# Performance work log

Measured on AMD Instinct MI355X. Metric: run time of the kernel, lower is better.

## Reference

```python
import jax, jax.numpy as jnp
import numpy as np

EPS = 1e-5
NUM_HEADS = 16


def _rmsnorm(x, w, eps=EPS):
    var = jnp.mean(jnp.square(x), axis=-1, keepdims=True)
    return x * jax.lax.rsqrt(var + eps) * w


def setup_inputs() -> dict:
    key = jax.random.key(0)
    ks = jax.random.split(key, 7)
    B, T, H = 4, 8192, 1024
    KD, VD = 512, 1024          # key_dim = 0.5*H, value_dim = H
    hk, hv = KD // NUM_HEADS, VD // NUM_HEADS  # 32, 64
    return {
        "hidden_states": jax.random.normal(ks[0], (B, T, H), jnp.float32),
        "recurrent_state": jax.random.normal(ks[1], (B, NUM_HEADS, hk, hv), jnp.float32),
        "norm_w": jax.random.uniform(ks[2], (H,), jnp.float32, 0.5, 1.5),
        "q_w": jax.random.normal(ks[3], (KD, H), jnp.float32) * 0.02,
        "v_norm_w": jax.random.uniform(ks[4], (hv,), jnp.float32, 0.5, 1.5),
        "o_w": jax.random.normal(ks[5], (H, VD), jnp.float32) * 0.02,
        "gate_w": jax.random.normal(ks[6], (H, H), jnp.float32) * 0.02,
    }


def reference(hidden_states, recurrent_state, norm_w, q_w, v_norm_w, o_w, gate_w):
    B, T, H = hidden_states.shape
    nh = NUM_HEADS
    x = _rmsnorm(hidden_states, norm_w)                      # [B,T,H]
    q = (x @ q_w.T).reshape(B, T, nh, -1)                    # [B,T,h,dk]
    # F.normalize(dim=-1): divide by max(L2 norm, 1e-12)
    q = q / jnp.maximum(jnp.linalg.norm(q, axis=-1, keepdims=True), 1e-12)
    o = jnp.einsum('bthk,bhkv->bthv', q, recurrent_state)    # [B,T,h,dv]
    o = _rmsnorm(o, v_norm_w)
    o = o.reshape(B, T, -1) @ o_w.T                          # [B,T,H]
    gate = jax.nn.sigmoid(x @ gate_w.T)                      # [B,T,H]
    return gate * o
```

## Files before the change

kernel.cpp:

```cpp
#include <hip/hip_runtime.h>
#include <hip/hip_bf16.h>
#include <stdint.h>

typedef __attribute__((ext_vector_type(8))) short short8;
typedef __attribute__((ext_vector_type(4))) float floatx4;
typedef __attribute__((ext_vector_type(2))) unsigned int uint2v;

#define DEV static __device__ __forceinline__
#define FENCE() asm volatile("" ::: "memory")

DEV unsigned short f2bs(float f) {
  union { float f; unsigned u; } v; v.f = f;
  unsigned u = v.u;
  u += 0x7fffu + ((u >> 16) & 1u);
  return (unsigned short)(u >> 16);
}
DEV float bs2f(unsigned short s) {
  union { unsigned u; float f; } v; v.u = ((unsigned)s) << 16;
  return v.f;
}
DEV unsigned pack2(float a, float b) {
  return (unsigned)f2bs(a) | ((unsigned)f2bs(b) << 16);
}

DEV void gload_lds16(const void* g, void* l) {
  __builtin_amdgcn_global_load_lds(
      (const __attribute__((address_space(1))) void*)g,
      (__attribute__((address_space(3))) void*)l, 16, 0, 0);
}

static constexpr int Hdim = 1024;
static constexpr int KDim = 512;
static constexpr int NH = 16;
static constexpr int HK = 32;
static constexpr int HV = 64;
static constexpr int Mtok = 4 * 8192;

__global__ __launch_bounds__(256) void k_cvt(const float4* __restrict__ in,
                                             uint2v* __restrict__ out, int n4) {
  int i = blockIdx.x * 256 + threadIdx.x;
  if (i >= n4) return;
  float4 v = in[i];
  uint2v o;
  o.x = pack2(v.x, v.y);
  o.y = pack2(v.z, v.w);
  out[i] = o;
}

__global__ __launch_bounds__(256) void k_cvts(const float* __restrict__ S,
                                              unsigned short* __restrict__ St) {
  int i = blockIdx.x * 256 + threadIdx.x;
  if (i >= 4 * NH * HV * HK) return;
  int k = i & 31, v = (i >> 5) & 63, bh = i >> 11;
  St[i] = f2bs(S[(size_t)(bh * HK + k) * HV + v]);
}

__global__ __launch_bounds__(256) void k_rmsnorm(const float* __restrict__ hs,
                                                 const float* __restrict__ nw,
                                                 uint2v* __restrict__ X) {
  const int token = blockIdx.x;
  const int tid = threadIdx.x;
  float4 h = ((const float4*)(hs + (size_t)token * Hdim))[tid];
  float ss = h.x * h.x + h.y * h.y + h.z * h.z + h.w * h.w;
#pragma unroll
  for (int off = 32; off > 0; off >>= 1) ss += __shfl_down(ss, off, 64);
  __shared__ float red[4];
  const int lane = tid & 63, wid = tid >> 6;
  if (lane == 0) red[wid] = ss;
  __syncthreads();
  float tot = red[0] + red[1] + red[2] + red[3];
  float sc = rsqrtf(tot * (1.0f / Hdim) + 1e-5f);
  float4 w = ((const float4*)nw)[tid];
  uint2v o;
  o.x = pack2(h.x * sc * w.x, h.y * sc * w.y);
  o.y = pack2(h.z * sc * w.z, h.w * sc * w.w);
  X[(size_t)token * 256 + tid] = o;
}

DEV void gemm128d(const unsigned short* __restrict__ A,
                  const unsigned short* __restrict__ Bw, const int K,
                  const int m0, const int n0, unsigned short* LDS,
                  floatx4 (&acc)[4][4], const int tid) {
  const int lane = tid & 63;
  const int w = tid >> 6;
  const int wr = w >> 1, wc = w & 1;
  const int frr = lane & 15;
  const int frk = (lane >> 4) * 8;
  const int aswz = (frr & 7) * 8;
  const int r_a = tid >> 3;
  const int c_src = ((tid & 7) ^ (r_a & 7)) * 8;
  const unsigned short* Ag = A + (size_t)(m0 + r_a) * K + c_src;
  const unsigned short* Bg = Bw + (size_t)(n0 + r_a) * K + c_src;
  const int NT = K >> 6;

  {
    char* AsD = (char*)LDS + tid * 16;
    char* BsD = (char*)(LDS + 16384) + tid * 16;
#pragma unroll
    for (int i = 0; i < 4; ++i) {
      gload_lds16(Ag + (size_t)i * 32 * K, AsD + i * 4096);
      gload_lds16(Bg + (size_t)i * 32 * K, BsD + i * 4096);
    }
  }
  asm volatile("s_waitcnt vmcnt(0)" ::: "memory");
  __builtin_amdgcn_s_barrier();
  FENCE();

  int cur = 0;
  for (int t = 0; t < NT; ++t) {
    if (t + 1 < NT) {
      char* AsD = (char*)(LDS + (cur ^ 1) * 8192) + tid * 16;
      char* BsD = (char*)(LDS + 16384 + (cur ^ 1) * 8192) + tid * 16;
      const int k0 = (t + 1) * 64;
#pragma unroll
      for (int i = 0; i < 4; ++i) {
        gload_lds16(Ag + (size_t)i * 32 * K + k0, AsD + i * 4096);
        gload_lds16(Bg + (size_t)i * 32 * K + k0, BsD + i * 4096);
      }
    }
    const unsigned short* Asb = LDS + cur * 8192;
    const unsigned short* Bsb = LDS + 16384 + cur * 8192;
#pragma unroll
    for (int kk = 0; kk < 2; ++kk) {
      short8 a[4], b[4];
#pragma unroll
      for (int mi = 0; mi < 4; ++mi)
        a[mi] = *(const short8*)
            &Asb[(wr * 64 + mi * 16 + frr) * 64 + ((kk * 32 + frk) ^ aswz)];
#pragma unroll
      for (int ni = 0; ni < 4; ++ni)
        b[ni] = *(const short8*)
            &Bsb[(wc * 64 + ni * 16 + frr) * 64 + ((kk * 32 + frk) ^ aswz)];
#pragma unroll
      for (int mi = 0; mi < 4; ++mi)
#pragma unroll
        for (int ni = 0; ni < 4; ++ni)
          acc[mi][ni] = __builtin_amdgcn_mfma_f32_16x16x32_bf16(
              a[mi], b[ni], acc[mi][ni], 0, 0, 0);
    }
    if (t + 1 < NT) {
      asm volatile("s_waitcnt vmcnt(0)" ::: "memory");
      __builtin_amdgcn_s_barrier();
      FENCE();
    }
    cur ^= 1;
  }
  __syncthreads();
}

__global__ __launch_bounds__(256, 2) void k_fused_go(
    const unsigned short* __restrict__ X, const unsigned short* __restrict__ Ob,
    const unsigned short* __restrict__ gwb,
    const unsigned short* __restrict__ owb, float* __restrict__ out) {
  __shared__ unsigned short LDS[4 * 128 * 64];
  const int tid = threadIdx.x;
  const int lane = tid & 63;
  const int w = tid >> 6;
  const int wr = w >> 1, wc = w & 1;
  const int bid = blockIdx.x;
  const int v = (bid & 7) * 256 + (bid >> 3);
  const int m0 = (v >> 3) * 128;
  const int n0 = (v & 7) * 128;

  floatx4 acc[4][4];
#pragma unroll
  for (int i = 0; i < 4; ++i)
#pragma unroll
    for (int j = 0; j < 4; ++j) acc[i][j] = (floatx4){0.f, 0.f, 0.f, 0.f};

  gemm128d(X, gwb, Hdim, m0, n0, LDS, acc, tid);

  unsigned pg[4][4][2];
#pragma unroll
  for (int mi = 0; mi < 4; ++mi)
#pragma unroll
    for (int ni = 0; ni < 4; ++ni) {
      float s0 = 1.0f / (1.0f + __expf(-acc[mi][ni][0]));
      float s1 = 1.0f / (1.0f + __expf(-acc[mi][ni][1]));
      float s2 = 1.0f / (1.0f + __expf(-acc[mi][ni][2]));
      float s3 = 1.0f / (1.0f + __expf(-acc[mi][ni][3]));
      pg[mi][ni][0] = pack2(s0, s1);
      pg[mi][ni][1] = pack2(s2, s3);
      acc[mi][ni] = (floatx4){0.f, 0.f, 0.f, 0.f};
    }

  gemm128d(Ob, owb, Hdim, m0, n0, LDS, acc, tid);

  const int rb = (lane >> 4) * 4;
#pragma unroll
  for (int mi = 0; mi < 4; ++mi)
#pragma unroll
    for (int ni = 0; ni < 4; ++ni) {
      const int n = n0 + wc * 64 + ni * 16 + (lane & 15);
#pragma unroll
      for (int r = 0; r < 4; ++r) {
        const int m = m0 + wr * 64 + mi * 16 + rb + r;
        float g = bs2f((unsigned short)(pg[mi][ni][r >> 1] >> ((r & 1) * 16)));
        out[(size_t)m * Hdim + n] = g * acc[mi][ni][r];
      }
    }
}

__global__ __launch_bounds__(256, 2) void k_fused_q(
    const unsigned short* __restrict__ X, const unsigned short* __restrict__ qwb,
    const unsigned short* __restrict__ St, const float* __restrict__ vnw,
    unsigned short* __restrict__ Ob) {
  __shared__ unsigned short LD[4 * 128 * 64];
  const int tid = threadIdx.x;
  const int lane = tid & 63;
  const int w = tid >> 6;
  const int wr = w >> 1, wc = w & 1;
  const int bid = blockIdx.x;
  const int v = (bid & 7) * 128 + (bid >> 3);
  const int m0 = (v >> 2) * 128;
  const int n0 = (v & 3) * 128;
  const int h0 = n0 >> 5;
  const int batch = m0 >> 13;

  floatx4 acc[4][4];
#pragma unroll
  for (int i = 0; i < 4; ++i)
#pragma unroll
    for (int j = 0; j < 4; ++j) acc[i][j] = (floatx4){0.f, 0.f, 0.f, 0.f};

  gemm128d(X, qwb, Hdim, m0, n0, LD, acc, tid);

  const int rb = (lane >> 4) * 4;
  const int frr = lane & 15;
#pragma unroll
  for (int mi = 0; mi < 4; ++mi)
#pragma unroll
    for (int p = 0; p < 2; ++p) {
#pragma unroll
      for (int r = 0; r < 4; ++r) {
        float v0 = acc[mi][2 * p][r], v1 = acc[mi][2 * p + 1][r];
        float ss = v0 * v0 + v1 * v1;
        ss += __shfl_xor(ss, 1, 64);
        ss += __shfl_xor(ss, 2, 64);
        ss += __shfl_xor(ss, 4, 64);
        ss += __shfl_xor(ss, 8, 64);
        const float inv = 1.0f / fmaxf(sqrtf(ss), 1e-12f);
        const int m = wr * 64 + mi * 16 + rb + r;
        const int c0 = wc * 64 + p * 32 + frr;
        const int sw = (m & 7) * 8;
        LD[m * 128 + (c0 ^ sw)] = f2bs(v0 * inv);
        LD[m * 128 + ((c0 + 16) ^ sw)] = f2bs(v1 * inv);
      }
    }
  __syncthreads();

  const int frk = (lane >> 4) * 8;
  float wv[4];
#pragma unroll
  for (int ni = 0; ni < 4; ++ni) wv[ni] = vnw[ni * 16 + frr];

#pragma unroll
  for (int hh = 0; hh < 4; ++hh) {
    const unsigned short* Sp = St + (size_t)(batch * NH + h0 + hh) * (HV * HK);
    short8 bfr[4];
#pragma unroll
    for (int ni = 0; ni < 4; ++ni)
      bfr[ni] = *(const short8*)&Sp[(ni * 16 + frr) * HK + frk];
    floatx4 acc2[2][4];
#pragma unroll
    for (int i = 0; i < 2; ++i)
#pragma unroll
      for (int j = 0; j < 4; ++j) acc2[i][j] = (floatx4){0.f, 0.f, 0.f, 0.f};
    short8 af[2];
#pragma unroll
    for (int mi2 = 0; mi2 < 2; ++mi2) {
      const int m = w * 32 + mi2 * 16 + frr;
      af[mi2] = *(const short8*)&LD[m * 128 + ((hh * 32 + frk) ^ ((m & 7) * 8))];
    }
#pragma unroll
    for (int mi2 = 0; mi2 < 2; ++mi2)
#pragma unroll
      for (int ni = 0; ni < 4; ++ni)
        acc2[mi2][ni] = __builtin_amdgcn_mfma_f32_16x16x32_bf16(
            af[mi2], bfr[ni], acc2[mi2][ni], 0, 0, 0);

#pragma unroll
    for (int mi2 = 0; mi2 < 2; ++mi2)
#pragma unroll
      for (int r = 0; r < 4; ++r) {
        float ss2 = 0.f;
#pragma unroll
        for (int ni = 0; ni < 4; ++ni) ss2 += acc2[mi2][ni][r] * acc2[mi2][ni][r];
        ss2 += __shfl_xor(ss2, 1, 64);
        ss2 += __shfl_xor(ss2, 2, 64);
        ss2 += __shfl_xor(ss2, 4, 64);
        ss2 += __shfl_xor(ss2, 8, 64);
        const float sc = rsqrtf(ss2 * (1.0f / HV) + 1e-5f);
        const int m = m0 + w * 32 + mi2 * 16 + rb + r;
        unsigned short* Op = Ob + (size_t)m * Hdim + (h0 + hh) * HV;
#pragma unroll
        for (int ni = 0; ni < 4; ++ni)
          Op[ni * 16 + frr] = f2bs(acc2[mi2][ni][r] * sc * wv[ni]);
      }
  }
}

extern "C" void kernel_launch(void* const* d_in, const int* in_sizes, int n_in,
                              void* d_out, int out_size, void* d_ws, size_t ws_size,
                              hipStream_t stream) {
  const float* hs = (const float*)d_in[0];
  const float* Srec = (const float*)d_in[1];
  const float* nw = (const float*)d_in[2];
  const float* qw = (const float*)d_in[3];
  const float* vnw = (const float*)d_in[4];
  const float* ow = (const float*)d_in[5];
  const float* gw = (const float*)d_in[6];

  char* ws = (char*)d_ws;
  unsigned short* X = (unsigned short*)(ws);
  unsigned short* Ob = (unsigned short*)(ws + ((size_t)64 << 20));
  unsigned short* qwb = (unsigned short*)(ws + ((size_t)128 << 20));
  unsigned short* gwb = (unsigned short*)(ws + ((size_t)129 << 20));
  unsigned short* owb = (unsigned short*)(ws + ((size_t)131 << 20));
  unsigned short* Stb = (unsigned short*)(ws + ((size_t)133 << 20));

  k_cvt<<<(KDim * Hdim / 4 + 255) / 256, 256, 0, stream>>>(
      (const float4*)qw, (uint2v*)qwb, KDim * Hdim / 4);
  k_cvt<<<(Hdim * Hdim / 4 + 255) / 256, 256, 0, stream>>>(
      (const float4*)gw, (uint2v*)gwb, Hdim * Hdim / 4);
  k_cvt<<<(Hdim * Hdim / 4 + 255) / 256, 256, 0, stream>>>(
      (const float4*)ow, (uint2v*)owb, Hdim * Hdim / 4);
  k_cvts<<<(4 * NH * HV * HK + 255) / 256, 256, 0, stream>>>(Srec, Stb);

  k_rmsnorm<<<Mtok, 256, 0, stream>>>(hs, nw, (uint2v*)X);

  k_fused_q<<<(Mtok / 128) * (KDim / 128), 256, 0, stream>>>(
      X, qwb, Stb, vnw, Ob);

  k_fused_go<<<(Mtok / 128) * (Hdim / 128), 256, 0, stream>>>(
      X, Ob, gwb, owb, (float*)d_out);
}
```

Baseline: 259.1 us.

## Merge weight conversion launches, wave-per-token rmsnorm, raise MFMA priority

Combines the three weight bf16 conversions and the state transpose into one prep kernel, cutting launch overhead. Rmsnorm now uses one wavefront per token with a xor-shuffle reduction, so the LDS reduction and block barrier go away. The GEMM inner loop raises wave priority around the MFMA block to favour matrix issue over loads from other waves. The priority change may help or hurt, depending on how well it overlaps with memory traffic.

Result: no change. 254.7 us (-1.7%).

```diff
diff --git a/kernel.cpp b/kernel.cpp
--- a/kernel.cpp
+++ b/kernel.cpp
@@ -36,10 +36,7 @@
 static constexpr int HV = 64;
 static constexpr int Mtok = 4 * 8192;
 
-__global__ __launch_bounds__(256) void k_cvt(const float4* __restrict__ in,
-                                             uint2v* __restrict__ out, int n4) {
-  int i = blockIdx.x * 256 + threadIdx.x;
-  if (i >= n4) return;
+DEV void cvt4(const float4* __restrict__ in, uint2v* __restrict__ out, int i) {
   float4 v = in[i];
   uint2v o;
   o.x = pack2(v.x, v.y);
@@ -47,10 +44,27 @@
   out[i] = o;
 }
 
-__global__ __launch_bounds__(256) void k_cvts(const float* __restrict__ S,
-                                              unsigned short* __restrict__ St) {
+__global__ __launch_bounds__(256) void k_prep(
+    const float* __restrict__ qw, const float* __restrict__ gw,
+    const float* __restrict__ ow, const float* __restrict__ S,
+    uint2v* __restrict__ qwb, uint2v* __restrict__ gwb,
+    uint2v* __restrict__ owb, unsigned short* __restrict__ St) {
   int i = blockIdx.x * 256 + threadIdx.x;
-  if (i >= 4 * NH * HV * HK) return;
+  if (i < 131072) {
+    cvt4((const float4*)qw, qwb, i);
+    return;
+  }
+  i -= 131072;
+  if (i < 262144) {
+    cvt4((const float4*)gw, gwb, i);
+    return;
+  }
+  i -= 262144;
+  if (i < 262144) {
+    cvt4((const float4*)ow, owb, i);
+    return;
+  }
+  i -= 262144;
   int k = i & 31, v = (i >> 5) & 63, bh = i >> 11;
   St[i] = f2bs(S[(size_t)(bh * HK + k) * HV + v]);
 }
@@ -58,23 +72,28 @@
 __global__ __launch_bounds__(256) void k_rmsnorm(const float* __restrict__ hs,
                                                  const float* __restrict__ nw,
                                                  uint2v* __restrict__ X) {
-  const int token = blockIdx.x;
-  const int tid = threadIdx.x;
-  float4 h = ((const float4*)(hs + (size_t)token * Hdim))[tid];
-  float ss = h.x * h.x + h.y * h.y + h.z * h.z + h.w * h.w;
-#pragma unroll
-  for (int off = 32; off > 0; off >>= 1) ss += __shfl_down(ss, off, 64);
-  __shared__ float red[4];
-  const int lane = tid & 63, wid = tid >> 6;
-  if (lane == 0) red[wid] = ss;
-  __syncthreads();
-  float tot = red[0] + red[1] + red[2] + red[3];
-  float sc = rsqrtf(tot * (1.0f / Hdim) + 1e-5f);
-  float4 w = ((const float4*)nw)[tid];
-  uint2v o;
-  o.x = pack2(h.x * sc * w.x, h.y * sc * w.y);
-  o.y = pack2(h.z * sc * w.z, h.w * sc * w.w);
-  X[(size_t)token * 256 + tid] = o;
+  const int lane = threadIdx.x & 63;
+  const int token = blockIdx.x * 4 + (threadIdx.x >> 6);
+  const float4* hp = (const float4*)(hs + (size_t)token * Hdim);
+  float4 h[4];
+  float ss = 0.f;
+#pragma unroll
+  for (int i = 0; i < 4; ++i) {
+    h[i] = hp[i * 64 + lane];
+    ss += h[i].x * h[i].x + h[i].y * h[i].y + h[i].z * h[i].z +
+          h[i].w * h[i].w;
+  }
+#pragma unroll
+  for (int off = 1; off < 64; off <<= 1) ss += __shfl_xor(ss, off, 64);
+  const float sc = rsqrtf(ss * (1.0f / Hdim) + 1e-5f);
+#pragma unroll
+  for (int i = 0; i < 4; ++i) {
+    float4 w = ((const float4*)nw)[i * 64 + lane];
+    uint2v o;
+    o.x = pack2(h[i].x * sc * w.x, h[i].y * sc * w.y);
+    o.y = pack2(h[i].z * sc * w.z, h[i].w * sc * w.w);
+    X[(size_t)token * 256 + i * 64 + lane] = o;
+  }
 }
 
 DEV void gemm128d(const unsigned short* __restrict__ A,
@@ -131,12 +150,14 @@
       for (int ni = 0; ni < 4; ++ni)
         b[ni] = *(const short8*)
             &Bsb[(wc * 64 + ni * 16 + frr) * 64 + ((kk * 32 + frk) ^ aswz)];
+      __builtin_amdgcn_s_setprio(1);
 #pragma unroll
       for (int mi = 0; mi < 4; ++mi)
 #pragma unroll
         for (int ni = 0; ni < 4; ++ni)
           acc[mi][ni] = __builtin_amdgcn_mfma_f32_16x16x32_bf16(
               a[mi], b[ni], acc[mi][ni], 0, 0, 0);
+      __builtin_amdgcn_s_setprio(0);
     }
     if (t + 1 < NT) {
       asm volatile("s_waitcnt vmcnt(0)" ::: "memory");
@@ -319,15 +340,10 @@
   unsigned short* owb = (unsigned short*)(ws + ((size_t)131 << 20));
   unsigned short* Stb = (unsigned short*)(ws + ((size_t)133 << 20));
 
-  k_cvt<<<(KDim * Hdim / 4 + 255) / 256, 256, 0, stream>>>(
-      (const float4*)qw, (uint2v*)qwb, KDim * Hdim / 4);
-  k_cvt<<<(Hdim * Hdim / 4 + 255) / 256, 256, 0, stream>>>(
-      (const float4*)gw, (uint2v*)gwb, Hdim * Hdim / 4);
-  k_cvt<<<(Hdim * Hdim / 4 + 255) / 256, 256, 0, stream>>>(
-      (const float4*)ow, (uint2v*)owb, Hdim * Hdim / 4);
-  k_cvts<<<(4 * NH * HV * HK + 255) / 256, 256, 0, stream>>>(Srec, Stb);
-
-  k_rmsnorm<<<Mtok, 256, 0, stream>>>(hs, nw, (uint2v*)X);
+  k_prep<<<3072, 256, 0, stream>>>(qw, gw, ow, Srec, (uint2v*)qwb,
+                                   (uint2v*)gwb, (uint2v*)owb, Stb);
+
+  k_rmsnorm<<<Mtok / 4, 256, 0, stream>>>(hs, nw, (uint2v*)X);
 
   k_fused_q<<<(Mtok / 128) * (KDim / 128), 256, 0, stream>>>(
       X, qwb, Stb, vnw, Ob);
```
